# Kernel optimization log

Hardware: AMD Instinct MI355X
Metric: run time of the kernel (lower is better)

Reference implementation:

```python
import jax, jax.numpy as jnp
import numpy as np

N_NODES = 10000
N_EDGES = 160000
DIM = 1024


def setup_inputs() -> dict:
    key = jax.random.key(0)
    k1, k2, k3 = jax.random.split(key, 3)
    x = jax.random.normal(k1, (N_NODES, DIM), dtype=jnp.float32)
    edge_index = jax.random.randint(k2, (2, N_EDGES), 0, N_NODES, dtype=jnp.int64)
    # Glorot-style init for the GCNConv weight; zero bias (PyG default)
    W = jax.random.normal(k3, (DIM, DIM), dtype=jnp.float32) * (1.0 / np.sqrt(DIM))
    b = jnp.zeros((DIM,), dtype=jnp.float32)
    return {"x": x, "edge_index": edge_index, "W": W, "b": b}


def reference(x, edge_index, W, b):
    """GCNConv (add_self_loops=True, symmetric norm) -> Dropout(eval=identity) -> ReLU."""
    n = x.shape[0]
    loops = jnp.arange(n, dtype=edge_index.dtype)
    src = jnp.concatenate([edge_index[0], loops])  # [E+N]
    dst = jnp.concatenate([edge_index[1], loops])  # [E+N]

    # symmetric normalization: deg^{-1/2}[src] * deg^{-1/2}[dst], deg on dst side
    deg = jax.ops.segment_sum(jnp.ones_like(dst, dtype=x.dtype), dst, num_segments=n)
    dinv = jnp.where(deg > 0, jax.lax.rsqrt(deg), jnp.zeros_like(deg))
    norm = dinv[src] * dinv[dst]  # [E+N]

    h = x @ W                                   # [N, D] dense transform first
    msg = h[src] * norm[:, None]                # gather + edge scaling [E+N, D]
    out = jax.ops.segment_sum(msg, dst, num_segments=n) + b  # scatter-add + bias

    # Dropout(0.5) is identity in eval mode; activation is ReLU
    return jax.nn.relu(out)
```

## Files before the change

### kernel.cpp

```cpp
#include <hip/hip_runtime.h>
#include <hip/hip_bf16.h>
#include <cstdint>
#include <cstddef>

typedef __bf16 bf16x8 __attribute__((ext_vector_type(8)));
typedef float  f32x4  __attribute__((ext_vector_type(4)));
typedef float  f32x2  __attribute__((ext_vector_type(2)));

#define D_DIM 1024
#define BM 128
#define BN 128
#define BK 64
#define NXCD 8
#define CAP 64

#define GLB(p) ((const __attribute__((address_space(1))) void*)(p))
#define LDS(p) ((__attribute__((address_space(3))) void*)(p))

__global__ __launch_bounds__(256) void prep_kernel(
    const float* __restrict__ x, __bf16* __restrict__ xb,
    const float* __restrict__ W, __bf16* __restrict__ wT,
    const int* __restrict__ ei, int* __restrict__ cnt, int* __restrict__ col,
    int N, int MP, int E, int nconv, int ntr)
{
    int blk = blockIdx.x, tid = threadIdx.x;
    if (blk < nconv) {
        int i = blk * 256 + tid;
        int total = MP * (D_DIM / 8);
        if (i >= total) return;
        int row = i >> 7;
        size_t base = (size_t)i * 8;
        bf16x8 o;
        if (row < N) {
            float4 v0 = *(const float4*)(x + base);
            float4 v1 = *(const float4*)(x + base + 4);
            o[0] = (__bf16)v0.x; o[1] = (__bf16)v0.y; o[2] = (__bf16)v0.z; o[3] = (__bf16)v0.w;
            o[4] = (__bf16)v1.x; o[5] = (__bf16)v1.y; o[6] = (__bf16)v1.z; o[7] = (__bf16)v1.w;
        } else {
            #pragma unroll
            for (int j = 0; j < 8; ++j) o[j] = (__bf16)0.f;
        }
        *(bf16x8*)(xb + base) = o;
    } else if (blk < nconv + ntr) {
        __shared__ float tile[32][33];
        int bb = blk - nconv;
        int nb = (bb & 31) * 32, kb = (bb >> 5) * 32;
        int tx = tid & 31, ty = tid >> 5;
        #pragma unroll
        for (int i = 0; i < 32; i += 8)
            tile[ty + i][tx] = W[(size_t)(kb + ty + i) * D_DIM + nb + tx];
        __syncthreads();
        #pragma unroll
        for (int i = 0; i < 32; i += 8)
            wT[(size_t)(nb + ty + i) * D_DIM + kb + tx] = (__bf16)tile[tx][ty + i];
    } else {
        int e = (blk - nconv - ntr) * 256 + tid;
        if (e < E) {
            const int* src = ei;
            const int* dst = ei + E;
            int d = dst[e];
            int pos = atomicAdd(&cnt[d], 1);
            if (pos < CAP) col[(d << 6) + pos] = src[e] << 11;
        }
    }
}

__global__ __launch_bounds__(256) void gemmpad_kernel(
    const __bf16* __restrict__ A,
    const __bf16* __restrict__ BT,
    __bf16* __restrict__ C,
    const int* __restrict__ cnt, int* __restrict__ col, int Nn,
    int mtiles, int ntiles, int chunk, int npad)
{
    int tid = threadIdx.x;
    if ((int)blockIdx.x < npad) {
        int d = blockIdx.x * 256 + tid;
        if (d < Nn) {
            int c  = min(cnt[d], CAP);
            int p1 = (c + 7) & ~7;
            int zoff = Nn << 11;
            for (int p = c; p < p1; ++p) col[(d << 6) + p] = zoff;
        }
        return;
    }
    __shared__ __bf16 As[BM * BK];
    __shared__ __bf16 Bs[BN * BK];

    int wg = blockIdx.x - npad;
    int c8 = wg & (NXCD - 1);
    int r  = wg >> 3;
    int bm = c8 * chunk + r / ntiles;
    int bn = r % ntiles;
    if (bm >= mtiles) return;

    int wid = tid >> 6, lane = tid & 63;
    int wr = wid >> 1, wc = wid & 1;

    f32x4 acc[4][4] = {};
    for (int ks = 0; ks < D_DIM / BK; ++ks) {
        #pragma unroll
        for (int i = 0; i < 4; ++i) {
            int c   = i * 256 + wid * 64 + lane;
            int row = c >> 3;
            int js  = (c & 7) ^ (row & 7);
            const __bf16* ga = A  + (size_t)(bm * BM + row) * D_DIM + ks * BK + js * 8;
            const __bf16* gb = BT + (size_t)(bn * BN + row) * D_DIM + ks * BK + js * 8;
            __builtin_amdgcn_global_load_lds(GLB(ga), LDS(As + c * 8), 16, 0, 0);
            __builtin_amdgcn_global_load_lds(GLB(gb), LDS(Bs + c * 8), 16, 0, 0);
        }
        asm volatile("s_waitcnt vmcnt(0)" ::: "memory");
        __syncthreads();
        #pragma unroll
        for (int kk = 0; kk < 2; ++kk) {
            bf16x8 af[4], bfr[4];
            int jgrp = kk * 4 + (lane >> 4);
            #pragma unroll
            for (int mi = 0; mi < 4; ++mi) {
                int rr = wr * 64 + mi * 16 + (lane & 15);
                af[mi] = *(const bf16x8*)(As + rr * BK + ((jgrp ^ (rr & 7)) << 3));
            }
            #pragma unroll
            for (int ni = 0; ni < 4; ++ni) {
                int rr = wc * 64 + ni * 16 + (lane & 15);
                bfr[ni] = *(const bf16x8*)(Bs + rr * BK + ((jgrp ^ (rr & 7)) << 3));
            }
            #pragma unroll
            for (int mi = 0; mi < 4; ++mi)
                #pragma unroll
                for (int ni = 0; ni < 4; ++ni)
                    acc[mi][ni] = __builtin_amdgcn_mfma_f32_16x16x32_bf16(
                        af[mi], bfr[ni], acc[mi][ni], 0, 0, 0);
        }
        __syncthreads();
    }

    #pragma unroll
    for (int mi = 0; mi < 4; ++mi)
        #pragma unroll
        for (int rr = 0; rr < 4; ++rr) {
            int row = bm * BM + wr * 64 + mi * 16 + (lane >> 4) * 4 + rr;
            float dvr = 0.0f;
            if (row < Nn) dvr = rsqrtf((float)min(cnt[row], CAP) + 1.0f);
            #pragma unroll
            for (int ni = 0; ni < 4; ++ni) {
                int colc = bn * BN + wc * 64 + ni * 16 + (lane & 15);
                C[(size_t)row * D_DIM + colc] = (__bf16)(acc[mi][ni][rr] * dvr);
            }
        }
}

__global__ __launch_bounds__(256) void scatter_kernel(
    const __bf16* __restrict__ h, const int* __restrict__ cnt,
    const int* __restrict__ col, const float* __restrict__ bias,
    float* __restrict__ out, int N)
{
    int blk = blockIdx.x;
    int c   = blk & (NXCD - 1);
    int q   = blk >> 3;
    int wid = threadIdx.x >> 6, lane = threadIdx.x & 63;
    int d = q * 4 + wid;
    if (d >= N) return;

    const char* hb = (const char*)h + (size_t)c * 256;
    int lane4 = lane * 4;

    uint32_t su = *(const uint32_t*)(hb + (((uint32_t)d << 11) + lane4));
    f32x2 a;
    a[0] = __uint_as_float(su << 16);
    a[1] = __uint_as_float(su & 0xffff0000u);

    int cdeg = min(cnt[d], CAP);
    int r0 = d << 6;
    int r1 = r0 + ((cdeg + 7) & ~7);
    for (int e = r0; e < r1; e += 8) {
        int4 c0 = *(const int4*)(col + e);
        int4 c1 = *(const int4*)(col + e + 4);
        uint32_t u[8];
        u[0] = *(const uint32_t*)(hb + ((uint32_t)c0.x + lane4));
        u[1] = *(const uint32_t*)(hb + ((uint32_t)c0.y + lane4));
        u[2] = *(const uint32_t*)(hb + ((uint32_t)c0.z + lane4));
        u[3] = *(const uint32_t*)(hb + ((uint32_t)c0.w + lane4));
        u[4] = *(const uint32_t*)(hb + ((uint32_t)c1.x + lane4));
        u[5] = *(const uint32_t*)(hb + ((uint32_t)c1.y + lane4));
        u[6] = *(const uint32_t*)(hb + ((uint32_t)c1.z + lane4));
        u[7] = *(const uint32_t*)(hb + ((uint32_t)c1.w + lane4));
        #pragma unroll
        for (int t = 0; t < 8; ++t) {
            f32x2 v;
            v[0] = __uint_as_float(u[t] << 16);
            v[1] = __uint_as_float(u[t] & 0xffff0000u);
            a += v;
        }
    }

    float dv = rsqrtf((float)cdeg + 1.0f);
    int cbase = c * 128 + lane * 2;
    f32x2 bb = *(const f32x2*)(bias + cbase);
    f32x2 o;
    o[0] = fmaxf(fmaf(a[0], dv, bb[0]), 0.f);
    o[1] = fmaxf(fmaf(a[1], dv, bb[1]), 0.f);
    __builtin_nontemporal_store(o, (f32x2*)(out + (size_t)d * D_DIM + cbase));
}

extern "C" void kernel_launch(void* const* d_in, const int* in_sizes, int n_in,
                              void* d_out, int out_size, void* d_ws, size_t ws_size,
                              hipStream_t stream)
{
    const float* x  = (const float*)d_in[0];
    const int*   ei = (const int*)d_in[1];
    const float* W  = (const float*)d_in[2];
    const float* b  = (const float*)d_in[3];
    float* out = (float*)d_out;

    const int N = in_sizes[0] / D_DIM;
    const int E = in_sizes[1] / 2;
    const int MP = ((N + BM - 1) / BM) * BM;

    char* ws = (char*)d_ws;
    size_t off = 0;
    auto alloc = [&](size_t bytes) -> char* {
        char* p = ws + off;
        off += (bytes + 255) & ~(size_t)255;
        return p;
    };
    __bf16* xb  = (__bf16*)alloc((size_t)MP * D_DIM * 2);
    __bf16* wT  = (__bf16*)alloc((size_t)D_DIM * D_DIM * 2);
    __bf16* h   = (__bf16*)alloc((size_t)MP * D_DIM * 2);
    int*    cnt = (int*)alloc((size_t)N * 4);
    int*    col = (int*)alloc((size_t)N * CAP * 4);
    (void)ws_size;

    (void)hipMemsetAsync(cnt, 0, (size_t)N * 4, stream);

    int nconv = (MP * (D_DIM / 8) + 255) / 256;
    int ntr   = (D_DIM / 32) * (D_DIM / 32);
    int ncnt  = (E + 255) / 256;
    prep_kernel<<<nconv + ntr + ncnt, 256, 0, stream>>>(x, xb, W, wT, ei,
                                                        cnt, col, N, MP, E,
                                                        nconv, ntr);

    int mtiles = MP / BM;
    int ntiles = D_DIM / BN;
    int chunk  = (mtiles + NXCD - 1) / NXCD;
    int ngem   = NXCD * chunk * ntiles;
    int npad   = (N + 255) / 256;
    gemmpad_kernel<<<npad + ngem, 256, 0, stream>>>(xb, wT, h, cnt, col, N,
                                                    mtiles, ntiles, chunk, npad);

    int sblocks = ((N + 3) / 4) * NXCD;
    scatter_kernel<<<sblocks, 256, 0, stream>>>(h, cnt, col, b, out, N);
}
```

Measured before the change: 108.7 us.

## Double-buffer GEMM LDS tiles with K-step 32 to overlap loads and MFMA

Splits the GEMM K loop into 32-wide steps with two LDS buffers per operand, so the next slice is loaded with global_load_lds while MFMAs run on the current one. The XOR swizzle is adapted to the 4-chunk rows. Total LDS use stays the same. The cost is twice as many barriers and loop iterations, and it relies on the end-of-loop barrier to wait for the outstanding loads.

```diff
diff --git a/kernel.cpp b/kernel.cpp
--- a/kernel.cpp
+++ b/kernel.cpp
@@ -10,7 +10,6 @@
 #define D_DIM 1024
 #define BM 128
 #define BN 128
-#define BK 64
 #define NXCD 8
 #define CAP 64
 
@@ -83,8 +82,8 @@
         }
         return;
     }
-    __shared__ __bf16 As[BM * BK];
-    __shared__ __bf16 Bs[BN * BK];
+    __shared__ __bf16 As[2][BM * 32];
+    __shared__ __bf16 Bs[2][BN * 32];
 
     int wg = blockIdx.x - npad;
     int c8 = wg & (NXCD - 1);
@@ -96,41 +95,46 @@
     int wid = tid >> 6, lane = tid & 63;
     int wr = wid >> 1, wc = wid & 1;
 
+    auto stage = [&](int h, int sel) {
+        #pragma unroll
+        for (int i = 0; i < 2; ++i) {
+            int c   = i * 256 + tid;
+            int row = c >> 2;
+            int js  = (c & 3) ^ (row & 3);
+            const __bf16* ga = A  + (size_t)(bm * BM + row) * D_DIM + h * 32 + js * 8;
+            const __bf16* gb = BT + (size_t)(bn * BN + row) * D_DIM + h * 32 + js * 8;
+            __builtin_amdgcn_global_load_lds(GLB(ga), LDS(&As[sel][c * 8]), 16, 0, 0);
+            __builtin_amdgcn_global_load_lds(GLB(gb), LDS(&Bs[sel][c * 8]), 16, 0, 0);
+        }
+    };
+
     f32x4 acc[4][4] = {};
-    for (int ks = 0; ks < D_DIM / BK; ++ks) {
-        #pragma unroll
-        for (int i = 0; i < 4; ++i) {
-            int c   = i * 256 + wid * 64 + lane;
-            int row = c >> 3;
-            int js  = (c & 7) ^ (row & 7);
-            const __bf16* ga = A  + (size_t)(bm * BM + row) * D_DIM + ks * BK + js * 8;
-            const __bf16* gb = BT + (size_t)(bn * BN + row) * D_DIM + ks * BK + js * 8;
-            __builtin_amdgcn_global_load_lds(GLB(ga), LDS(As + c * 8), 16, 0, 0);
-            __builtin_amdgcn_global_load_lds(GLB(gb), LDS(Bs + c * 8), 16, 0, 0);
-        }
-        asm volatile("s_waitcnt vmcnt(0)" ::: "memory");
-        __syncthreads();
-        #pragma unroll
-        for (int kk = 0; kk < 2; ++kk) {
-            bf16x8 af[4], bfr[4];
-            int jgrp = kk * 4 + (lane >> 4);
+    stage(0, 0);
+    asm volatile("s_waitcnt vmcnt(0)" ::: "memory");
+    __syncthreads();
+
+    const int halves = D_DIM / 32;
+    for (int h = 0; h < halves; ++h) {
+        int cur = h & 1;
+        if (h + 1 < halves) stage(h + 1, cur ^ 1);
+        bf16x8 af[4], bfr[4];
+        int j = lane >> 4;
+        #pragma unroll
+        for (int mi = 0; mi < 4; ++mi) {
+            int rr = wr * 64 + mi * 16 + (lane & 15);
+            af[mi] = *(const bf16x8*)(&As[cur][rr * 32 + ((j ^ (rr & 3)) << 3)]);
+        }
+        #pragma unroll
+        for (int ni = 0; ni < 4; ++ni) {
+            int rr = wc * 64 + ni * 16 + (lane & 15);
+            bfr[ni] = *(const bf16x8*)(&Bs[cur][rr * 32 + ((j ^ (rr & 3)) << 3)]);
+        }
+        #pragma unroll
+        for (int mi = 0; mi < 4; ++mi)
             #pragma unroll
-            for (int mi = 0; mi < 4; ++mi) {
-                int rr = wr * 64 + mi * 16 + (lane & 15);
-                af[mi] = *(const bf16x8*)(As + rr * BK + ((jgrp ^ (rr & 7)) << 3));
-            }
-            #pragma unroll
-            for (int ni = 0; ni < 4; ++ni) {
-                int rr = wc * 64 + ni * 16 + (lane & 15);
-                bfr[ni] = *(const bf16x8*)(Bs + rr * BK + ((jgrp ^ (rr & 7)) << 3));
-            }
-            #pragma unroll
-            for (int mi = 0; mi < 4; ++mi)
-                #pragma unroll
-                for (int ni = 0; ni < 4; ++ni)
-                    acc[mi][ni] = __builtin_amdgcn_mfma_f32_16x16x32_bf16(
-                        af[mi], bfr[ni], acc[mi][ni], 0, 0, 0);
-        }
+            for (int ni = 0; ni < 4; ++ni)
+                acc[mi][ni] = __builtin_amdgcn_mfma_f32_16x16x32_bf16(
+                    af[mi], bfr[ni], acc[mi][ni], 0, 0, 0);
         __syncthreads();
     }
 
```

Result: faster. 101.1 us (-7.0%).
